# Performance work log

Hardware: AMD Instinct MI355X
Metric: run time of the kernel (lower is better)

Reference implementation:

```python
import jax, jax.numpy as jnp
from jax import lax
import numpy as np

DN = ('NCHW', 'OIHW', 'NCHW')

def _conv(x, w, b, s):
    # torch Conv2d(kernel=3, padding=1, stride=s)
    y = lax.conv_general_dilated(x, w, (s, s), ((1, 1), (1, 1)), dimension_numbers=DN)
    return y + b[None, :, None, None]

def _convT(x, w, b, s):
    # torch ConvTranspose2d weight layout [in, out, kh, kw]; kernel=3, padding=1, output_padding=s-1
    wk = jnp.flip(w, (2, 3)).transpose(1, 0, 2, 3)  # -> OIHW
    y = lax.conv_general_dilated(x, wk, (1, 1), ((1, s), (1, s)), lhs_dilation=(s, s), dimension_numbers=DN)
    return y + b[None, :, None, None]

def _inorm(x, eps=1e-5):
    # torch InstanceNorm2d (affine=False)
    m = jnp.mean(x, (2, 3), keepdims=True)
    v = jnp.var(x, (2, 3), keepdims=True)
    return (x - m) * lax.rsqrt(v + eps)

def _prelu(x, a):
    return jnp.where(x >= 0, x, a * x)

def _block(x, w, b, a, s):
    return _prelu(_inorm(_conv(x, w, b, s)), a)

def _sage(x, src, tgt, wl, bl, wr, n):
    # PyG SAGEConv, mean aggregation: lin_l(scatter_mean(x[src] -> tgt)) + lin_r(x)
    deg = jnp.zeros((n,), x.dtype).at[tgt].add(1.0)
    agg = jnp.zeros((x.shape[0], n, x.shape[2]), x.dtype).at[:, tgt].add(x[:, src])
    agg = agg / jnp.maximum(deg, 1.0)[None, :, None]
    return jnp.einsum('bnc,oc->bno', agg, wl) + bl + jnp.einsum('bnc,oc->bno', x, wr)

def setup_inputs() -> dict:
    keys = iter(jax.random.split(jax.random.key(0), 64))
    def rn(shape, s=0.05):
        return jax.random.normal(next(keys), shape, jnp.float32) * s
    inp = {}
    inp['x'] = jax.random.normal(next(keys), (16, 1, 400, 400), jnp.float32)
    inp['edges'] = jax.random.randint(next(keys), (2, 5000), 0, 625, jnp.int32)
    for name, (ci, co) in zip(['d4', 'd3', 'd2', 'd1'], [(1, 32), (32, 64), (64, 128), (128, 256)]):
        inp['w_' + name] = rn((co, ci, 3, 3)); inp['b_' + name] = rn((co,))
        inp['a_' + name] = jnp.full((1,), 0.25, jnp.float32)
    inp['w_bot'] = rn((256, 256, 3, 3)); inp['b_bot'] = rn((256,))
    inp['a_bot'] = jnp.full((1,), 0.25, jnp.float32)
    for i in ['1', '2']:
        inp['wl' + i] = rn((256, 256)); inp['bl' + i] = rn((256,)); inp['wr' + i] = rn((256, 256))
    for name, (ci, co) in zip(['u1', 'u2', 'u3'], [(512, 128), (256, 64), (128, 32)]):
        inp['w_' + name] = rn((ci, co, 3, 3)); inp['b_' + name] = rn((co,))
        inp['a_' + name] = jnp.full((1,), 0.25, jnp.float32)
    inp['w_u4'] = rn((64, 2, 3, 3)); inp['b_u4'] = rn((2,))
    return inp

def reference(x, edges, w_d4, b_d4, a_d4, w_d3, b_d3, a_d3, w_d2, b_d2, a_d2, w_d1, b_d1, a_d1, w_bot, b_bot, a_bot, wl1, bl1, wr1, wl2, bl2, wr2, w_u1, b_u1, a_u1, w_u2, b_u2, a_u2, w_u3, b_u3, a_u3, w_u4, b_u4):
    xs = []
    x = _block(x, w_d4, b_d4, a_d4, 2); xs.append(x)   # [B,32,200,200]
    x = _block(x, w_d3, b_d3, a_d3, 2); xs.append(x)   # [B,64,100,100]
    x = _block(x, w_d2, b_d2, a_d2, 2); xs.append(x)   # [B,128,50,50]
    x = _block(x, w_d1, b_d1, a_d1, 2); xs.append(x)   # [B,256,25,25]
    x = _block(x, w_bot, b_bot, a_bot, 1)              # [B,256,25,25]
    B = x.shape[0]
    x = x.reshape(B, 256, -1).transpose(0, 2, 1)       # [B,625,256]
    src, tgt = edges[0], edges[1]
    x = jax.nn.relu(_sage(x, src, tgt, wl1, bl1, wr1, 625))
    x = jax.nn.relu(_sage(x, src, tgt, wl2, bl2, wr2, 625))
    x = x.transpose(0, 2, 1).reshape(B, 256, 25, 25)
    x = jnp.concatenate([xs[3], x], 1)                 # 512 ch
    x = _prelu(_inorm(_convT(x, w_u1, b_u1, 2)), a_u1) # [B,128,50,50]
    x = jnp.concatenate([xs[2], x], 1)
    x = _prelu(_inorm(_convT(x, w_u2, b_u2, 2)), a_u2) # [B,64,100,100]
    x = jnp.concatenate([xs[1], x], 1)
    x = _prelu(_inorm(_convT(x, w_u3, b_u3, 2)), a_u3) # [B,32,200,200]
    x = jnp.concatenate([xs[0], x], 1)
    return _convT(x, w_u4, b_u4, 2)                    # [B,2,400,400], conv_only top
```

## Files before the change

kernel.cpp:

```cpp
#include <hip/hip_runtime.h>
#include <hip/hip_bf16.h>

typedef __hip_bfloat16 bf16;

typedef __bf16 bf16x8 __attribute__((ext_vector_type(8)));
typedef float  f32x16 __attribute__((ext_vector_type(16)));

static __device__ __forceinline__ float bf(const bf16 v){ return __bfloat162float(v); }
static __device__ __forceinline__ float bfu(unsigned short u){
  unsigned fw = ((unsigned)u) << 16; float v; __builtin_memcpy(&v, &fw, 4); return v;
}

static __device__ __forceinline__ float ldm(const void* p, long i, int f){
  return f ? ((const float*)p)[i] : __bfloat162float(((const bf16*)p)[i]);
}
static __device__ __forceinline__ void stm(void* p, long i, int f, float v){
  if(f) ((float*)p)[i] = v; else ((bf16*)p)[i] = __float2bfloat16(v);
}
static __device__ __forceinline__ unsigned short bfbits(float v){
  __hip_bfloat16 h = __float2bfloat16(v);
  return *(unsigned short*)&h;
}

__global__ void k_detect(const void* __restrict__ w, int* __restrict__ mode){
  if(blockIdx.x == 0 && threadIdx.x == 0){
    const unsigned int* u = (const unsigned int*)w;
    int saneLo = 0;
    for(int i = 0; i < 64; i++){
      unsigned short lo = (unsigned short)(u[i] & 0xFFFFu);
      unsigned int fw = ((unsigned int)lo) << 16;
      float v; __builtin_memcpy(&v, &fw, 4);
      float a = fabsf(v);
      if(a > 1e-7f && a < 100.f) saneLo++;
    }
    *mode = (saneLo >= 48) ? 0 : 1;
  }
}

__global__ void k_wtrans6(const void* __restrict__ w, bf16* __restrict__ wF,
                          const int* __restrict__ dmode){
  int idx = blockIdx.x * 256 + threadIdx.x;
  if(idx >= 65536) return;
  int dm = *dmode;
  int e = idx & 7;
  int L = (idx >> 3) & 63;
  int r = idx >> 9;
  int nc = r & 7;
  int kc = r >> 3;
  int o = nc*32 + (L & 31);
  int c = kc*16 + (L >> 5)*8 + e;
  wF[idx] = __float2bfloat16(ldm(w, (long)o*256 + c, dm));
}

__global__ void k_wtrans4(const void* __restrict__ w, bf16* __restrict__ wF,
                          const int* __restrict__ dmode, int Cin, int Cout){
  int idx = blockIdx.x * 256 + threadIdx.x;
  if(idx >= Cin * Cout * 9) return;
  int dm = *dmode;
  int e = idx & 7;
  int L = (idx >> 3) & 63;
  int r = idx >> 9;
  int NC = Cout >> 5;
  int nc = r % NC; r /= NC;
  int t  = r % 9;
  int kc = r / 9;
  int ci = kc*16 + (L>>5)*8 + e;
  int co = nc*32 + (L&31);
  wF[idx] = __float2bfloat16(ldm(w, ((long)ci*Cout + co)*9 + t, dm));
}

__global__ void k_wtrans5(const void* __restrict__ w, bf16* __restrict__ wF,
                          const int* __restrict__ dmode, int Cin, int Cout){
  int idx = blockIdx.x * 256 + threadIdx.x;
  if(idx >= Cin * Cout * 9) return;
  int dm = *dmode;
  int e = idx & 7;
  int L = (idx >> 3) & 63;
  int r = idx >> 9;
  int NC = Cout >> 5;
  int nc = r % NC; r /= NC;
  int t  = r % 9;
  int kc = r / 9;
  int ci = kc*16 + (L>>5)*8 + e;
  int co = nc*32 + (L&31);
  wF[idx] = __float2bfloat16(ldm(w, ((long)co*Cin + ci)*9 + t, dm));
}

__global__ __launch_bounds__(256, 4)
void k_conv_d4(const void* __restrict__ in, long in_off,
               const void* __restrict__ w, const void* __restrict__ bias,
               bf16* __restrict__ out, const int* __restrict__ dmode)
{
  __shared__ float sW[288];
  __shared__ float sB[32];
  int tid = threadIdx.x;
  int dm = *dmode;
  for(int e = tid; e < 288; e += 256) sW[e] = ldm(w, e, dm);
  if(tid < 32)  sB[tid] = ldm(bias, tid, dm);
  __syncthreads();
  int r = tid / 50, jt = tid % 50;
  if(r >= 5) return;
  int ho = blockIdx.x * 5 + r;
  int b  = blockIdx.z;
  int j0 = jt * 4;

  float x[3][9];
  long ibase = in_off + (long)b * 160000;
  #pragma unroll
  for(int rr = 0; rr < 3; rr++){
    int ir = 2*ho - 1 + rr;
    if(ir < 0 || ir >= 400){
      #pragma unroll
      for(int c = 0; c < 9; c++) x[rr][c] = 0.f;
      continue;
    }
    long rb = ibase + (long)ir * 400;
    int c0 = 2*j0 - 1;
    #pragma unroll
    for(int c = 0; c < 9; c++){
      int ic = c0 + c;
      x[rr][c] = (ic >= 0 && ic < 400) ? ldm(in, rb + ic, dm) : 0.f;
    }
  }

  long obase = ((long)b * 32) * 40000 + (long)ho * 200 + j0;
  for(int co = 0; co < 32; co++){
    const float* wv = &sW[co*9];
    float bv = sB[co];
    float a[4];
    #pragma unroll
    for(int p = 0; p < 4; p++){
      float s = bv;
      #pragma unroll
      for(int kh = 0; kh < 3; kh++)
        #pragma unroll
        for(int kw = 0; kw < 3; kw++)
          s += x[kh][2*p + kw] * wv[kh*3 + kw];
      a[p] = s;
    }
    ushort4 pk;
    pk.x = bfbits(a[0]); pk.y = bfbits(a[1]); pk.z = bfbits(a[2]); pk.w = bfbits(a[3]);
    *(ushort4*)&out[obase + (long)co * 40000] = pk;
  }
}

template<int CW, int NWC, int NWM, int S, int OCC>
__global__ __launch_bounds__(256, OCC)
void k_convSM(const void* __restrict__ in, long in_off, int fin_sel,
              const bf16* __restrict__ wF, const void* __restrict__ bias,
              void* __restrict__ out, int fout,
              const int* __restrict__ dmode,
              int Cin, int Hin, int Win, int Cout, int Hout, int Wout, int nym)
{
  constexpr int CP = 40;
  constexpr int HALF = CW/2;
  __shared__ unsigned short sX[3*CW*CP];
  int tid  = threadIdx.x;
  int lane = tid & 63;
  int wv   = tid >> 6;
  int nc   = wv % NWC;
  int mt   = wv / NWC;
  int ho   = blockIdx.x;
  int colg = blockIdx.y % nym;
  int cog  = blockIdx.y / nym;
  int b    = blockIdx.z;
  int dm   = *dmode;
  int fin  = (fin_sel == 2) ? dm : fin_sel;
  int NCtot = Cout >> 5;
  int chunk = cog*NWC + nc;
  int jl   = mt*32 + (lane & 31);
  int hi   = lane >> 5;
  int C0   = S*(colg*NWM*32);
  int ir0  = S*ho - 1;

  f32x16 acc;
  #pragma unroll
  for(int q = 0; q < 16; q++) acc[q] = 0.f;

  int p0, p1, p2;
  if(S == 2){ p0 = jl; p1 = HALF + jl; p2 = jl + 1; }
  else      { p0 = jl; p1 = jl + 1;    p2 = jl + 2; }

  for(int ci0 = 0; ci0 < Cin; ci0 += 32){
    for(int e = tid; e < 12*CW; e += 256){
      int c  = e % CW;
      int s  = e / CW;
      int kg = s & 3, r = s >> 2;
      int ir = ir0 + r;
      int ic = C0 - 1 + c;
      unsigned pk0, pk1, pk2, pk3;
      if(ir >= 0 && ir < Hin && ic >= 0 && ic < Win){
        long step = (long)Hin*Win;
        long base = in_off + ((long)b*Cin + ci0 + kg*8)*step + (long)ir*Win + ic;
        unsigned short t8[8];
        #pragma unroll
        for(int u = 0; u < 8; u++) t8[u] = bfbits(ldm(in, base + u*step, fin));
        pk0 = t8[0] | ((unsigned)t8[1]<<16);
        pk1 = t8[2] | ((unsigned)t8[3]<<16);
        pk2 = t8[4] | ((unsigned)t8[5]<<16);
        pk3 = t8[6] | ((unsigned)t8[7]<<16);
      } else { pk0=0; pk1=0; pk2=0; pk3=0; }
      int pos = (S == 2) ? ((c&1) ? HALF + (c>>1) : (c>>1)) : c;
      uint4 q; q.x=pk0; q.y=pk1; q.z=pk2; q.w=pk3;
      *(uint4*)&sX[(r*CW + pos)*CP + kg*8] = q;
    }
    __syncthreads();

    #pragma unroll
    for(int kg2 = 0; kg2 < 2; kg2++){
      int kbase = 8*hi + kg2*16;
      bf16x8 x[9];
      #pragma unroll
      for(int r = 0; r < 3; r++){
        x[r*3+0] = *(const bf16x8*)&sX[(r*CW + p0)*CP + kbase];
        x[r*3+1] = *(const bf16x8*)&sX[(r*CW + p1)*CP + kbase];
        x[r*3+2] = *(const bf16x8*)&sX[(r*CW + p2)*CP + kbase];
      }
      int kc = (ci0 >> 4) + kg2;
      const bf16x8* wb = ((const bf16x8*)wF) + ((long)(kc*9)*NCtot + chunk)*64 + lane;
      const long ws = (long)NCtot*64;
      #pragma unroll
      for(int t = 0; t < 9; t++){
        bf16x8 w = wb[(long)t*ws];
        acc = __builtin_amdgcn_mfma_f32_32x32x16_bf16(w, x[t], acc, 0,0,0);
      }
    }
    __syncthreads();
  }

  int j = colg*NWM*32 + jl;
  if(j < Wout){
    #pragma unroll
    for(int r16 = 0; r16 < 16; r16++){
      int co = chunk*32 + (r16&3) + 8*(r16>>2) + 4*hi;
      float bv = ldm(bias, co, dm);
      stm(out, ((long)b*Cout + co)*Hout*Wout + (long)ho*Wout + j, fout, acc[r16] + bv);
    }
  }
}

__global__ void k_inorm_prelu(void* __restrict__ x, int f, int HW,
                              const void* __restrict__ a, const int* __restrict__ dmode)
{
  int dm = *dmode;
  long base = (long)blockIdx.x * HW;
  float s = 0.f, s2 = 0.f;
  int vec = (f == 0) && ((HW & 3) == 0);
  if(vec){
    const ushort4* vp = (const ushort4*)((const bf16*)x + base);
    int n = HW >> 2;
    for(int i = threadIdx.x; i < n; i += 256){
      ushort4 v = vp[i];
      float a0 = bfu(v.x), a1 = bfu(v.y), a2 = bfu(v.z), a3 = bfu(v.w);
      s  += (a0 + a1) + (a2 + a3);
      s2 += (a0*a0 + a1*a1) + (a2*a2 + a3*a3);
    }
  } else {
    for(int i = threadIdx.x; i < HW; i += 256){ float v = ldm(x, base + i, f); s += v; s2 += v*v; }
  }
  __shared__ float sh[256], sh2[256];
  sh[threadIdx.x] = s; sh2[threadIdx.x] = s2; __syncthreads();
  for(int off = 128; off > 0; off >>= 1){
    if(threadIdx.x < off){ sh[threadIdx.x] += sh[threadIdx.x+off]; sh2[threadIdx.x] += sh2[threadIdx.x+off]; }
    __syncthreads();
  }
  float mean = sh[0] / HW;
  float var  = sh2[0] / HW - mean * mean;
  float inv  = rsqrtf(fmaxf(var, 0.f) + 1e-5f);
  float alpha = ldm(a, 0, dm);
  if(vec){
    ushort4* vp = (ushort4*)((bf16*)x + base);
    int n = HW >> 2;
    for(int i = threadIdx.x; i < n; i += 256){
      ushort4 v = vp[i];
      float t[4] = { bfu(v.x), bfu(v.y), bfu(v.z), bfu(v.w) };
      #pragma unroll
      for(int k = 0; k < 4; k++){
        float u = (t[k] - mean) * inv;
        t[k] = u >= 0.f ? u : alpha * u;
      }
      ushort4 o;
      o.x = bfbits(t[0]); o.y = bfbits(t[1]); o.z = bfbits(t[2]); o.w = bfbits(t[3]);
      vp[i] = o;
    }
  } else {
    for(int i = threadIdx.x; i < HW; i += 256){
      float v = (ldm(x, base + i, f) - mean) * inv;
      stm(x, base + i, f, v >= 0.f ? v : alpha * v);
    }
  }
}

__global__ void k_transpose(const float* __restrict__ in, float* __restrict__ out, int B, int C, int N){
  long idx = (long)blockIdx.x * 256 + threadIdx.x;
  long total = (long)B * C * N; if(idx >= total) return;
  int c = (int)(idx % C); long t = idx / C; int n = (int)(t % N); int b = (int)(t / N);
  out[idx] = in[((long)b * C + c) * N + n];
}

__global__ void k_deg(const int* __restrict__ tgt, float* __restrict__ deg, int E){
  int e = blockIdx.x * 256 + threadIdx.x;
  if(e < E) atomicAdd(&deg[tgt[e]], 1.0f);
}

__global__ void k_scatter(const float* __restrict__ xT, const int* __restrict__ src,
                          const int* __restrict__ tgt, float* __restrict__ agg,
                          int E, int C, int N, int B)
{
  int t = blockIdx.x * 256 + threadIdx.x;
  if(t >= E * C) return;
  int c = t % C; int e = t / C;
  int s = src[e], d = tgt[e];
  for(int b = 0; b < B; b++){
    atomicAdd(&agg[((long)b * N + d) * C + c], xT[((long)b * N + s) * C + c]);
  }
}

__global__ __launch_bounds__(256, 4)
void k_sageM(const float* __restrict__ xT, const float* __restrict__ agg,
             const float* __restrict__ deg,
             const bf16* __restrict__ wlF, const bf16* __restrict__ wrF,
             const void* __restrict__ bl,
             float* __restrict__ out, const int* __restrict__ dmode,
             int NROW, int trans)
{
  constexpr int CP = 264;
  __shared__ unsigned short sS[2*32*CP];
  int tid  = threadIdx.x;
  int lane = tid & 63;
  int wv   = tid >> 6;
  int ln   = lane & 31;
  int hi   = lane >> 5;
  int n0   = blockIdx.x * 32;
  int og0  = blockIdx.y * 128;
  int ncg  = blockIdx.y*4 + wv;
  int dm   = *dmode;

  for(int e = tid; e < 4096; e += 256){
    int c4 = e & 63;
    int r  = (e >> 6) & 31;
    int ar = e >> 11;
    int row = n0 + r;
    unsigned pk0 = 0, pk1 = 0;
    if(row < NROW){
      const float* sp = ar ? agg : xT;
      float4 v = *(const float4*)&sp[(long)row*256 + c4*4];
      if(ar){
        int n = row % 625;
        float dinv = 1.0f / fmaxf(deg[n], 1.0f);
        v.x *= dinv; v.y *= dinv; v.z *= dinv; v.w *= dinv;
      }
      pk0 = bfbits(v.x) | ((unsigned)bfbits(v.y) << 16);
      pk1 = bfbits(v.z) | ((unsigned)bfbits(v.w) << 16);
    }
    uint2 q; q.x = pk0; q.y = pk1;
    *(uint2*)&sS[(ar*32 + r)*CP + c4*4] = q;
  }
  __syncthreads();

  f32x16 acc;
  #pragma unroll
  for(int q = 0; q < 16; q++) acc[q] = 0.f;

  int xb = ln*CP + 8*hi;
  #pragma unroll
  for(int kc = 0; kc < 16; kc++){
    bf16x8 bx = *(const bf16x8*)&sS[xb + kc*16];
    bf16x8 ba = *(const bf16x8*)&sS[32*CP + xb + kc*16];
    bf16x8 wl = ((const bf16x8*)wlF)[(long)(kc*8 + ncg)*64 + lane];
    bf16x8 wr = ((const bf16x8*)wrF)[(long)(kc*8 + ncg)*64 + lane];
    acc = __builtin_amdgcn_mfma_f32_32x32x16_bf16(wl, ba, acc, 0,0,0);
    acc = __builtin_amdgcn_mfma_f32_32x32x16_bf16(wr, bx, acc, 0,0,0);
  }

  if(trans){
    int row = n0 + ln;
    if(row < NROW){
      int b = row / 625, n = row - b*625;
      #pragma unroll
      for(int r16 = 0; r16 < 16; r16++){
        int o = ncg*32 + (r16&3) + 8*(r16>>2) + 4*hi;
        float v = acc[r16] + ldm(bl, o, dm);
        out[((long)b*256 + o)*625 + n] = fmaxf(v, 0.f);
      }
    }
  } else {
    float* sO = (float*)sS;
    __syncthreads();
    #pragma unroll
    for(int r16 = 0; r16 < 16; r16++){
      int ol = wv*32 + (r16&3) + 8*(r16>>2) + 4*hi;
      float v = acc[r16] + ldm(bl, og0 + ol, dm);
      sO[ln*130 + ol] = fmaxf(v, 0.f);
    }
    __syncthreads();
    for(int e = tid; e < 4096; e += 256){
      int r = e >> 7, oc = e & 127;
      int row = n0 + r;
      if(row < NROW) out[(long)row*256 + og0 + oc] = sO[r*130 + oc];
    }
  }
}

template<int CW, int NWC, int CC, int CIP, int OCC>
__global__ __launch_bounds__(256, OCC)
void k_convTF(const void* __restrict__ inA, int fA,
              const void* __restrict__ inB, int fB,
              const bf16* __restrict__ wF, const void* __restrict__ bias,
              bf16* __restrict__ out, const int* __restrict__ dmode,
              int Hin, int Win, int Cout)
{
  __shared__ unsigned short sX[2*CW*CIP];
  int tid  = threadIdx.x;
  int lane = tid & 63;
  int wv   = tid >> 6;
  int nc   = wv % NWC;
  int mt   = wv / NWC;
  int j0   = mt * 32;
  int i    = blockIdx.x;
  int b    = blockIdx.z;
  int dm   = *dmode;
  int ln   = lane & 31;
  int hi   = lane >> 5;
  int NCtot = Cout >> 5;

  f32x16 acc0, acc1, acc2, acc3;
  #pragma unroll
  for(int q = 0; q < 16; q++){ acc0[q]=0.f; acc1[q]=0.f; acc2[q]=0.f; acc3[q]=0.f; }

  #pragma unroll
  for(int half = 0; half < 2; half++){
    const void* sp = half ? inB : inA;
    int ff = half ? fB : fA;
    for(int e = tid; e < 2*CW*(CC/8); e += 256){
      int col = e % CW;
      int s   = e / CW;
      int kg  = s % (CC/8);
      int row = s / (CC/8);
      int ii  = i + row;
      unsigned pk0=0, pk1=0, pk2=0, pk3=0;
      if(ii < Hin && col < Win){
        long step = (long)Hin*Win;
        long base = ((long)b*CC + kg*8)*step + (long)ii*Win + col;
        unsigned short t8[8];
        #pragma unroll
        for(int u = 0; u < 8; u++) t8[u] = bfbits(ldm(sp, base + u*step, ff));
        pk0 = t8[0] | ((unsigned)t8[1]<<16);
        pk1 = t8[2] | ((unsigned)t8[3]<<16);
        pk2 = t8[4] | ((unsigned)t8[5]<<16);
        pk3 = t8[6] | ((unsigned)t8[7]<<16);
      }
      uint4 q; q.x=pk0; q.y=pk1; q.z=pk2; q.w=pk3;
      *(uint4*)&sX[(row*CW + col)*CIP + kg*8] = q;
    }
    __syncthreads();

    for(int kc = 0; kc < CC/16; kc++){
      int kb = kc*16 + 8*hi;
      bf16x8 x00 = *(const bf16x8*)&sX[(j0 + ln)*CIP + kb];
      bf16x8 x01 = *(const bf16x8*)&sX[(j0 + ln + 1)*CIP + kb];
      bf16x8 x10 = *(const bf16x8*)&sX[(CW + j0 + ln)*CIP + kb];
      bf16x8 x11 = *(const bf16x8*)&sX[(CW + j0 + ln + 1)*CIP + kb];
      int kcg = half*(CC/16) + kc;
      const bf16x8* wb = ((const bf16x8*)wF) + ((long)(kcg*9)*NCtot + nc)*64 + lane;
      const int ws = NCtot*64;
      bf16x8 w0=wb[0],    w1=wb[ws],   w2=wb[2*ws], w3=wb[3*ws], w4=wb[4*ws],
             w5=wb[5*ws], w6=wb[6*ws], w7=wb[7*ws], w8=wb[8*ws];
      acc0 = __builtin_amdgcn_mfma_f32_32x32x16_bf16(w4, x00, acc0, 0,0,0);
      acc1 = __builtin_amdgcn_mfma_f32_32x32x16_bf16(w5, x00, acc1, 0,0,0);
      acc1 = __builtin_amdgcn_mfma_f32_32x32x16_bf16(w3, x01, acc1, 0,0,0);
      acc2 = __builtin_amdgcn_mfma_f32_32x32x16_bf16(w7, x00, acc2, 0,0,0);
      acc2 = __builtin_amdgcn_mfma_f32_32x32x16_bf16(w1, x10, acc2, 0,0,0);
      acc3 = __builtin_amdgcn_mfma_f32_32x32x16_bf16(w8, x00, acc3, 0,0,0);
      acc3 = __builtin_amdgcn_mfma_f32_32x32x16_bf16(w6, x01, acc3, 0,0,0);
      acc3 = __builtin_amdgcn_mfma_f32_32x32x16_bf16(w2, x10, acc3, 0,0,0);
      acc3 = __builtin_amdgcn_mfma_f32_32x32x16_bf16(w0, x11, acc3, 0,0,0);
    }
    __syncthreads();
  }

  int j = j0 + ln;
  if(j < Win){
    int Wout = 2*Win;
    #pragma unroll
    for(int r = 0; r < 16; r++){
      int co = nc*32 + (r&3) + 8*(r>>2) + 4*hi;
      float bv = ldm(bias, co, dm);
      long base0 = (((long)b*Cout + co)*2*Hin + 2*i)*(long)Wout + 2*j;
      unsigned p0 = bfbits(acc0[r]+bv) | ((unsigned)bfbits(acc1[r]+bv) << 16);
      unsigned p1 = bfbits(acc2[r]+bv) | ((unsigned)bfbits(acc3[r]+bv) << 16);
      *(unsigned*)&out[base0]        = p0;
      *(unsigned*)&out[base0 + Wout] = p1;
    }
  }
}

__global__ __launch_bounds__(256, 2)
void k_convT8(const bf16* __restrict__ inA, const bf16* __restrict__ inB,
              const void* __restrict__ w, const void* __restrict__ bias,
              void* __restrict__ out, long out_off, int fout_sel,
              const int* __restrict__ dmode, int Hin, int Win)
{
  __shared__ float sW[64*2*9];
  __shared__ float sB[2];
  int tid = threadIdx.x;
  int dm = *dmode;
  for(int e = tid; e < 64*2*9; e += 256) sW[e] = ldm(w, e, dm);
  if(tid < 2) sB[tid] = ldm(bias, tid, dm);
  __syncthreads();
  int r  = tid / 50;
  int jt = tid % 50;
  if(r >= 5) return;
  int i  = blockIdx.x * 5 + r;
  int b  = blockIdx.z;
  int j0 = jt * 4;
  int fout = (fout_sel == 2) ? dm : fout_sel;

  float acc[2][4][4];
  #pragma unroll
  for(int co = 0; co < 2; co++)
    #pragma unroll
    for(int p = 0; p < 4; p++){
      acc[co][p][0]=0.f; acc[co][p][1]=0.f; acc[co][p][2]=0.f; acc[co][p][3]=0.f;
    }

  bool e4   = (j0 + 4 < Win);
  bool row1 = (i + 1 < Hin);

  for(int ci = 0; ci < 64; ci++){
    const bf16* src = (ci < 32) ? inA : inB;
    int cc = ci & 31;
    const bf16* rp = src + ((long)b*32 + cc)*(long)Hin*Win + (long)i*Win + j0;
    float x0[5], x1[5];
    ushort4 v0 = *(const ushort4*)rp;
    x0[0]=bfu(v0.x); x0[1]=bfu(v0.y); x0[2]=bfu(v0.z); x0[3]=bfu(v0.w);
    x0[4] = e4 ? bf(rp[4]) : 0.f;
    if(row1){
      ushort4 v1 = *(const ushort4*)(rp + Win);
      x1[0]=bfu(v1.x); x1[1]=bfu(v1.y); x1[2]=bfu(v1.z); x1[3]=bfu(v1.w);
      x1[4] = e4 ? bf(rp[Win + 4]) : 0.f;
    } else {
      x1[0]=0.f; x1[1]=0.f; x1[2]=0.f; x1[3]=0.f; x1[4]=0.f;
    }
    const float* wp = &sW[ci*18];
    float wv[18];
    #pragma unroll
    for(int k = 0; k < 18; k++) wv[k] = wp[k];
    #pragma unroll
    for(int p = 0; p < 4; p++){
      float a00 = x0[p], a01 = x0[p+1], a10 = x1[p], a11 = x1[p+1];
      #pragma unroll
      for(int co = 0; co < 2; co++){
        const float* wc = &wv[co*9];
        acc[co][p][0] += a00*wc[4];
        acc[co][p][1] += a00*wc[5] + a01*wc[3];
        acc[co][p][2] += a00*wc[7] + a10*wc[1];
        acc[co][p][3] += a00*wc[8] + a01*wc[6] + a10*wc[2] + a11*wc[0];
      }
    }
  }
  int Wout = 2*Win;
  #pragma unroll
  for(int co = 0; co < 2; co++){
    float bv = sB[co];
    long base = out_off + (((long)b*2 + co)*2*Hin + 2*i)*(long)Wout + 2*j0;
    #pragma unroll
    for(int p = 0; p < 4; p++){
      stm(out, base + 2*p,            fout, acc[co][p][0] + bv);
      stm(out, base + 2*p + 1,        fout, acc[co][p][1] + bv);
      stm(out, base + 2*p + Wout,     fout, acc[co][p][2] + bv);
      stm(out, base + 2*p + Wout + 1, fout, acc[co][p][3] + bv);
    }
  }
}

static inline int cdiv(long a, long b){ return (int)((a + b - 1) / b); }

extern "C" void kernel_launch(void* const* d_in, const int* in_sizes, int n_in,
                              void* d_out, int out_size, void* d_ws, size_t ws_size,
                              hipStream_t stream) {
  const void* x_in  = d_in[0];
  const int*  edges = (const int*)d_in[1];
  const int* src = edges;
  const int* tgt = edges + 5000;
  const void *w_d4=d_in[2],  *b_d4=d_in[3],  *a_d4=d_in[4];
  const void *w_d3=d_in[5],  *b_d3=d_in[6],  *a_d3=d_in[7];
  const void *w_d2=d_in[8],  *b_d2=d_in[9],  *a_d2=d_in[10];
  const void *w_d1=d_in[11], *b_d1=d_in[12], *a_d1=d_in[13];
  const void *w_bot=d_in[14],*b_bot=d_in[15],*a_bot=d_in[16];
  const void *wl1=d_in[17], *bl1=d_in[18], *wr1=d_in[19];
  const void *wl2=d_in[20], *bl2=d_in[21], *wr2=d_in[22];
  const void *w_u1=d_in[23], *b_u1=d_in[24], *a_u1=d_in[25];
  const void *w_u2=d_in[26], *b_u2=d_in[27], *a_u2=d_in[28];
  const void *w_u3=d_in[29], *b_u3=d_in[30], *a_u3=d_in[31];
  const void *w_u4=d_in[32], *b_u4=d_in[33];

  const int NNODE = 625, E = 5000, CG = 256;

  const long TAIL = 4096 + 4*262144L + (589824L + 147456L + 36864L) * 2;
  const long ENCW = 976896L * 2;
  int Bc = 16;
  while(Bc > 1 && (7680000L * Bc + TAIL) > (long)ws_size) Bc >>= 1;
  int enc_in_pool = (Bc >= 8);
  if(!enc_in_pool){
    Bc = 16;
    while(Bc > 1 && (7680000L * Bc + TAIL + ENCW) > (long)ws_size) Bc >>= 1;
  }

  char* wsb = (char*)d_ws;
  long o_xs1  = 2560000L * Bc;
  long o_BIGA = 3840000L * Bc;
  long o_BIGB = 6400000L * Bc;
  long o_deg  = 7680000L * Bc;
  bf16*  xs0 = (bf16*)wsb;
  bf16*  xs1 = (bf16*)(wsb + o_xs1);
  bf16*  xs2 = (bf16*)(wsb + o_BIGA);
  bf16*  xs3 = (bf16*)(wsb + o_BIGA +  640000L*Bc);
  float* bot = (float*)(wsb + o_BIGA +  960000L*Bc);
  float* xT  = (float*)(wsb + o_BIGA + 1600000L*Bc);
  bf16*  u1  = (bf16*)(wsb + o_BIGA + 1600000L*Bc);
  bf16*  u3  = (bf16*)(wsb + o_BIGA);
  float* agg = (float*)(wsb + o_BIGB);
  float* g1  = (float*)(wsb + o_BIGB +  640000L*Bc);
  bf16*  u2  = (bf16*)(wsb + o_BIGB);
  float* deg = (float*)(wsb + o_deg);
  int*  mode = (int*)(wsb + o_deg + 3072);
  bf16*  wlF1 = (bf16*)(wsb + o_deg + 4096);
  bf16*  wrF1 = wlF1 + 65536;
  bf16*  wlF2 = wrF1 + 65536;
  bf16*  wrF2 = wlF2 + 65536;
  bf16*  wTu1 = (bf16*)(wsb + o_deg + 4096 + 4*262144L);
  bf16*  wTu2 = wTu1 + 589824;
  bf16*  wTu3 = wTu2 + 147456;
  bf16*  wTd3 = enc_in_pool ? (bf16*)(wsb + o_BIGA + 2240000L*Bc) : (wTu3 + 36864);
  bf16*  wTd2 = wTd3 + 18432;
  bf16*  wTd1 = wTd2 + 73728;
  bf16*  wTdB = wTd1 + 294912;
  float* g2  = bot;

  hipLaunchKernelGGL(k_detect, dim3(1), dim3(1), 0, stream, w_d4, mode);

  hipMemsetAsync(deg, 0, NNODE*sizeof(float), stream);
  hipLaunchKernelGGL(k_deg, dim3(cdiv(E,256)), dim3(256), 0, stream, tgt, deg, E);
  hipLaunchKernelGGL(k_wtrans6, dim3(256), dim3(256), 0, stream, wl1, wlF1, mode);
  hipLaunchKernelGGL(k_wtrans6, dim3(256), dim3(256), 0, stream, wr1, wrF1, mode);
  hipLaunchKernelGGL(k_wtrans6, dim3(256), dim3(256), 0, stream, wl2, wlF2, mode);
  hipLaunchKernelGGL(k_wtrans6, dim3(256), dim3(256), 0, stream, wr2, wrF2, mode);
  hipLaunchKernelGGL(k_wtrans4, dim3(cdiv(589824,256)), dim3(256), 0, stream, w_u1, wTu1, mode, 512, 128);
  hipLaunchKernelGGL(k_wtrans4, dim3(cdiv(147456,256)), dim3(256), 0, stream, w_u2, wTu2, mode, 256, 64);
  hipLaunchKernelGGL(k_wtrans4, dim3(cdiv(36864,256)),  dim3(256), 0, stream, w_u3, wTu3, mode, 128, 32);

  for(int bo = 0; bo < 16; bo += Bc){
    long x_off   = (long)bo * 160000;
    long out_off = (long)bo * 320000;

    hipLaunchKernelGGL(k_wtrans5, dim3(cdiv(18432,256)),  dim3(256), 0, stream, w_d3, wTd3, mode, 32, 64);
    hipLaunchKernelGGL(k_wtrans5, dim3(cdiv(73728,256)),  dim3(256), 0, stream, w_d2, wTd2, mode, 64, 128);
    hipLaunchKernelGGL(k_wtrans5, dim3(cdiv(294912,256)), dim3(256), 0, stream, w_d1, wTd1, mode, 128, 256);
    hipLaunchKernelGGL(k_wtrans5, dim3(cdiv(589824,256)), dim3(256), 0, stream, w_bot, wTdB, mode, 256, 256);

    hipLaunchKernelGGL(k_conv_d4, dim3(40, 1, Bc), dim3(256), 0, stream,
                       x_in, x_off, w_d4, b_d4, xs0, mode);
    hipLaunchKernelGGL(k_inorm_prelu, dim3(Bc*32), dim3(256), 0, stream, xs0, 0, 40000, a_d4, mode);
    hipLaunchKernelGGL((k_convSM<130,2,2,2,4>), dim3(100, 2, Bc), dim3(256), 0, stream,
                       xs0, 0L, 0, wTd3, b_d3, xs1, 0, mode, 32, 200, 200, 64, 100, 100, 2);
    hipLaunchKernelGGL(k_inorm_prelu, dim3(Bc*64), dim3(256), 0, stream, xs1, 0, 10000, a_d3, mode);
    hipLaunchKernelGGL((k_convSM<66,4,1,2,4>), dim3(50, 2, Bc), dim3(256), 0, stream,
                       xs1, 0L, 0, wTd2, b_d2, xs2, 0, mode, 64, 100, 100, 128, 50, 50, 2);
    hipLaunchKernelGGL(k_inorm_prelu, dim3(Bc*128), dim3(256), 0, stream, xs2, 0, 2500, a_d2, mode);
    hipLaunchKernelGGL((k_convSM<66,4,1,2,4>), dim3(25, 2, Bc), dim3(256), 0, stream,
                       xs2, 0L, 0, wTd1, b_d1, xs3, 0, mode, 128, 50, 50, 256, 25, 25, 1);
    hipLaunchKernelGGL(k_inorm_prelu, dim3(Bc*256), dim3(256), 0, stream, xs3, 0, 625, a_d1, mode);
    hipLaunchKernelGGL((k_convSM<34,4,1,1,4>), dim3(25, 2, Bc), dim3(256), 0, stream,
                       xs3, 0L, 0, wTdB, b_bot, bot, 1, mode, 256, 25, 25, 256, 25, 25, 1);
    hipLaunchKernelGGL(k_inorm_prelu, dim3(Bc*256), dim3(256), 0, stream, bot, 1, 625, a_bot, mode);

    { long n = (long)Bc*CG*NNODE;
      hipLaunchKernelGGL(k_transpose, dim3(cdiv(n,256)), dim3(256), 0, stream, bot, xT, Bc, CG, NNODE); }
    hipMemsetAsync(agg, 0, 640000L*Bc, stream);
    hipLaunchKernelGGL(k_scatter, dim3(cdiv((long)E*CG,256)), dim3(256), 0, stream, xT, src, tgt, agg, E, CG, NNODE, Bc);
    hipLaunchKernelGGL(k_sageM, dim3(cdiv((long)Bc*NNODE,32), 2), dim3(256), 0, stream,
                       xT, agg, deg, wlF1, wrF1, bl1, g1, mode, Bc*NNODE, 0);
    hipMemsetAsync(agg, 0, 640000L*Bc, stream);
    hipLaunchKernelGGL(k_scatter, dim3(cdiv((long)E*CG,256)), dim3(256), 0, stream, g1, src, tgt, agg, E, CG, NNODE, Bc);
    hipLaunchKernelGGL(k_sageM, dim3(cdiv((long)Bc*NNODE,32), 2), dim3(256), 0, stream,
                       g1, agg, deg, wlF2, wrF2, bl2, g2, mode, Bc*NNODE, 1);

    hipLaunchKernelGGL((k_convTF<34,4,256,264,4>), dim3(25, 1, Bc), dim3(256), 0, stream,
                       xs3, 0, g2, 1, wTu1, b_u1, u1, mode, 25, 25, 128);
    hipLaunchKernelGGL(k_inorm_prelu, dim3(Bc*128), dim3(256), 0, stream, u1, 0, 2500, a_u1, mode);
    hipLaunchKernelGGL((k_convTF<66,2,128,136,4>), dim3(50, 1, Bc), dim3(256), 0, stream,
                       xs2, 0, u1, 0, wTu2, b_u2, u2, mode, 50, 50, 64);
    hipLaunchKernelGGL(k_inorm_prelu, dim3(Bc*64), dim3(256), 0, stream, u2, 0, 10000, a_u2, mode);
    hipLaunchKernelGGL((k_convTF<130,1,64,72,4>), dim3(100, 1, Bc), dim3(256), 0, stream,
                       xs1, 0, u2, 0, wTu3, b_u3, u3, mode, 100, 100, 32);
    hipLaunchKernelGGL(k_inorm_prelu, dim3(Bc*32), dim3(256), 0, stream, u3, 0, 40000, a_u3, mode);
    hipLaunchKernelGGL(k_convT8, dim3(40, 1, Bc), dim3(256), 0, stream,
                       xs0, u3, w_u4, b_u4, d_out, out_off, 2, mode, 200, 200);
  }
}
```

Before: 905.6 us.

## Split convT channel halves across wave groups with LDS reduction

Transposed-conv kernel now uses 512 threads. Wave groups 0-3 process the skip-connection input channels and waves 4-7 the decoder input channels concurrently. Partial accumulators are then summed through shared memory before the bias and store. This aims to increase parallelism and remove the serialized two-phase staging. In exchange it doubles shared memory per block and adds a reduction pass.

```diff
diff --git a/kernel.cpp b/kernel.cpp
--- a/kernel.cpp
+++ b/kernel.cpp
@@ -402,20 +402,22 @@
   }
 }
 
-template<int CW, int NWC, int CC, int CIP, int OCC>
-__global__ __launch_bounds__(256, OCC)
-void k_convTF(const void* __restrict__ inA, int fA,
+template<int CW, int NWC, int NWM, int CC, int CIP>
+__global__ __launch_bounds__(512, 4)
+void k_convTG(const void* __restrict__ inA, int fA,
               const void* __restrict__ inB, int fB,
               const bf16* __restrict__ wF, const void* __restrict__ bias,
               bf16* __restrict__ out, const int* __restrict__ dmode,
               int Hin, int Win, int Cout)
 {
-  __shared__ unsigned short sX[2*CW*CIP];
+  __shared__ unsigned short sX[4*CW*CIP];
   int tid  = threadIdx.x;
   int lane = tid & 63;
   int wv   = tid >> 6;
-  int nc   = wv % NWC;
-  int mt   = wv / NWC;
+  int low  = wv & 3;
+  int h    = wv >> 2;
+  int nc   = low % NWC;
+  int mt   = low / NWC;
   int j0   = mt * 32;
   int i    = blockIdx.x;
   int b    = blockIdx.z;
@@ -428,69 +430,87 @@
   #pragma unroll
   for(int q = 0; q < 16; q++){ acc0[q]=0.f; acc1[q]=0.f; acc2[q]=0.f; acc3[q]=0.f; }
 
-  #pragma unroll
-  for(int half = 0; half < 2; half++){
-    const void* sp = half ? inB : inA;
-    int ff = half ? fB : fA;
-    for(int e = tid; e < 2*CW*(CC/8); e += 256){
-      int col = e % CW;
-      int s   = e / CW;
-      int kg  = s % (CC/8);
-      int row = s / (CC/8);
-      int ii  = i + row;
-      unsigned pk0=0, pk1=0, pk2=0, pk3=0;
-      if(ii < Hin && col < Win){
-        long step = (long)Hin*Win;
-        long base = ((long)b*CC + kg*8)*step + (long)ii*Win + col;
-        unsigned short t8[8];
-        #pragma unroll
-        for(int u = 0; u < 8; u++) t8[u] = bfbits(ldm(sp, base + u*step, ff));
-        pk0 = t8[0] | ((unsigned)t8[1]<<16);
-        pk1 = t8[2] | ((unsigned)t8[3]<<16);
-        pk2 = t8[4] | ((unsigned)t8[5]<<16);
-        pk3 = t8[6] | ((unsigned)t8[7]<<16);
+  for(int e = tid; e < 4*CW*(CC/8); e += 512){
+    int col = e % CW;
+    int s   = e / CW;
+    int kg  = s % (CC/8); s /= (CC/8);
+    int row = s & 1;
+    int hf  = s >> 1;
+    int ii  = i + row;
+    unsigned pk0=0, pk1=0, pk2=0, pk3=0;
+    if(ii < Hin && col < Win){
+      const void* sp = hf ? inB : inA;
+      int ff = hf ? fB : fA;
+      long step = (long)Hin*Win;
+      long base = ((long)b*CC + kg*8)*step + (long)ii*Win + col;
+      unsigned short t8[8];
+      #pragma unroll
+      for(int u = 0; u < 8; u++) t8[u] = bfbits(ldm(sp, base + u*step, ff));
+      pk0 = t8[0] | ((unsigned)t8[1]<<16);
+      pk1 = t8[2] | ((unsigned)t8[3]<<16);
+      pk2 = t8[4] | ((unsigned)t8[5]<<16);
+      pk3 = t8[6] | ((unsigned)t8[7]<<16);
+    }
+    uint4 q; q.x=pk0; q.y=pk1; q.z=pk2; q.w=pk3;
+    *(uint4*)&sX[((hf*2 + row)*CW + col)*CIP + kg*8] = q;
+  }
+  __syncthreads();
+
+  for(int kc = 0; kc < CC/16; kc++){
+    int kb = kc*16 + 8*hi;
+    bf16x8 x00 = *(const bf16x8*)&sX[((h*2+0)*CW + j0 + ln)*CIP + kb];
+    bf16x8 x01 = *(const bf16x8*)&sX[((h*2+0)*CW + j0 + ln + 1)*CIP + kb];
+    bf16x8 x10 = *(const bf16x8*)&sX[((h*2+1)*CW + j0 + ln)*CIP + kb];
+    bf16x8 x11 = *(const bf16x8*)&sX[((h*2+1)*CW + j0 + ln + 1)*CIP + kb];
+    int kcg = h*(CC/16) + kc;
+    const bf16x8* wb = ((const bf16x8*)wF) + ((long)(kcg*9)*NCtot + nc)*64 + lane;
+    const int ws = NCtot*64;
+    bf16x8 w0=wb[0],    w1=wb[ws],   w2=wb[2*ws], w3=wb[3*ws], w4=wb[4*ws],
+           w5=wb[5*ws], w6=wb[6*ws], w7=wb[7*ws], w8=wb[8*ws];
+    acc0 = __builtin_amdgcn_mfma_f32_32x32x16_bf16(w4, x00, acc0, 0,0,0);
+    acc1 = __builtin_amdgcn_mfma_f32_32x32x16_bf16(w5, x00, acc1, 0,0,0);
+    acc1 = __builtin_amdgcn_mfma_f32_32x32x16_bf16(w3, x01, acc1, 0,0,0);
+    acc2 = __builtin_amdgcn_mfma_f32_32x32x16_bf16(w7, x00, acc2, 0,0,0);
+    acc2 = __builtin_amdgcn_mfma_f32_32x32x16_bf16(w1, x10, acc2, 0,0,0);
+    acc3 = __builtin_amdgcn_mfma_f32_32x32x16_bf16(w8, x00, acc3, 0,0,0);
+    acc3 = __builtin_amdgcn_mfma_f32_32x32x16_bf16(w6, x01, acc3, 0,0,0);
+    acc3 = __builtin_amdgcn_mfma_f32_32x32x16_bf16(w2, x10, acc3, 0,0,0);
+    acc3 = __builtin_amdgcn_mfma_f32_32x32x16_bf16(w0, x11, acc3, 0,0,0);
+  }
+
+  float* sR = (float*)sX;
+  __syncthreads();
+  if(h == 1){
+    #pragma unroll
+    for(int q = 0; q < 16; q++){
+      sR[(0*16+q)*256 + low*64 + lane] = acc0[q];
+      sR[(1*16+q)*256 + low*64 + lane] = acc1[q];
+      sR[(2*16+q)*256 + low*64 + lane] = acc2[q];
+      sR[(3*16+q)*256 + low*64 + lane] = acc3[q];
+    }
+  }
+  __syncthreads();
+  if(h == 0){
+    #pragma unroll
+    for(int q = 0; q < 16; q++){
+      acc0[q] += sR[(0*16+q)*256 + low*64 + lane];
+      acc1[q] += sR[(1*16+q)*256 + low*64 + lane];
+      acc2[q] += sR[(2*16+q)*256 + low*64 + lane];
+      acc3[q] += sR[(3*16+q)*256 + low*64 + lane];
+    }
+    int j = j0 + ln;
+    if(j < Win){
+      int Wout = 2*Win;
+      #pragma unroll
+      for(int r = 0; r < 16; r++){
+        int co = nc*32 + (r&3) + 8*(r>>2) + 4*hi;
+        float bv = ldm(bias, co, dm);
+        long base0 = (((long)b*Cout + co)*2*Hin + 2*i)*(long)Wout + 2*j;
+        unsigned p0 = bfbits(acc0[r]+bv) | ((unsigned)bfbits(acc1[r]+bv) << 16);
+        unsigned p1 = bfbits(acc2[r]+bv) | ((unsigned)bfbits(acc3[r]+bv) << 16);
+        *(unsigned*)&out[base0]        = p0;
+        *(unsigned*)&out[base0 + Wout] = p1;
       }
-      uint4 q; q.x=pk0; q.y=pk1; q.z=pk2; q.w=pk3;
-      *(uint4*)&sX[(row*CW + col)*CIP + kg*8] = q;
-    }
-    __syncthreads();
-
-    for(int kc = 0; kc < CC/16; kc++){
-      int kb = kc*16 + 8*hi;
-      bf16x8 x00 = *(const bf16x8*)&sX[(j0 + ln)*CIP + kb];
-      bf16x8 x01 = *(const bf16x8*)&sX[(j0 + ln + 1)*CIP + kb];
-      bf16x8 x10 = *(const bf16x8*)&sX[(CW + j0 + ln)*CIP + kb];
-      bf16x8 x11 = *(const bf16x8*)&sX[(CW + j0 + ln + 1)*CIP + kb];
-      int kcg = half*(CC/16) + kc;
-      const bf16x8* wb = ((const bf16x8*)wF) + ((long)(kcg*9)*NCtot + nc)*64 + lane;
-      const int ws = NCtot*64;
-      bf16x8 w0=wb[0],    w1=wb[ws],   w2=wb[2*ws], w3=wb[3*ws], w4=wb[4*ws],
-             w5=wb[5*ws], w6=wb[6*ws], w7=wb[7*ws], w8=wb[8*ws];
-      acc0 = __builtin_amdgcn_mfma_f32_32x32x16_bf16(w4, x00, acc0, 0,0,0);
-      acc1 = __builtin_amdgcn_mfma_f32_32x32x16_bf16(w5, x00, acc1, 0,0,0);
-      acc1 = __builtin_amdgcn_mfma_f32_32x32x16_bf16(w3, x01, acc1, 0,0,0);
-      acc2 = __builtin_amdgcn_mfma_f32_32x32x16_bf16(w7, x00, acc2, 0,0,0);
-      acc2 = __builtin_amdgcn_mfma_f32_32x32x16_bf16(w1, x10, acc2, 0,0,0);
-      acc3 = __builtin_amdgcn_mfma_f32_32x32x16_bf16(w8, x00, acc3, 0,0,0);
-      acc3 = __builtin_amdgcn_mfma_f32_32x32x16_bf16(w6, x01, acc3, 0,0,0);
-      acc3 = __builtin_amdgcn_mfma_f32_32x32x16_bf16(w2, x10, acc3, 0,0,0);
-      acc3 = __builtin_amdgcn_mfma_f32_32x32x16_bf16(w0, x11, acc3, 0,0,0);
-    }
-    __syncthreads();
-  }
-
-  int j = j0 + ln;
-  if(j < Win){
-    int Wout = 2*Win;
-    #pragma unroll
-    for(int r = 0; r < 16; r++){
-      int co = nc*32 + (r&3) + 8*(r>>2) + 4*hi;
-      float bv = ldm(bias, co, dm);
-      long base0 = (((long)b*Cout + co)*2*Hin + 2*i)*(long)Wout + 2*j;
-      unsigned p0 = bfbits(acc0[r]+bv) | ((unsigned)bfbits(acc1[r]+bv) << 16);
-      unsigned p1 = bfbits(acc2[r]+bv) | ((unsigned)bfbits(acc3[r]+bv) << 16);
-      *(unsigned*)&out[base0]        = p0;
-      *(unsigned*)&out[base0 + Wout] = p1;
     }
   }
 }
@@ -686,13 +706,13 @@
     hipLaunchKernelGGL(k_sageM, dim3(cdiv((long)Bc*NNODE,32), 2), dim3(256), 0, stream,
                        g1, agg, deg, wlF2, wrF2, bl2, g2, mode, Bc*NNODE, 1);
 
-    hipLaunchKernelGGL((k_convTF<34,4,256,264,4>), dim3(25, 1, Bc), dim3(256), 0, stream,
+    hipLaunchKernelGGL((k_convTG<34,4,1,256,264>), dim3(25, 1, Bc), dim3(512), 0, stream,
                        xs3, 0, g2, 1, wTu1, b_u1, u1, mode, 25, 25, 128);
     hipLaunchKernelGGL(k_inorm_prelu, dim3(Bc*128), dim3(256), 0, stream, u1, 0, 2500, a_u1, mode);
-    hipLaunchKernelGGL((k_convTF<66,2,128,136,4>), dim3(50, 1, Bc), dim3(256), 0, stream,
+    hipLaunchKernelGGL((k_convTG<66,2,2,128,136>), dim3(50, 1, Bc), dim3(512), 0, stream,
                        xs2, 0, u1, 0, wTu2, b_u2, u2, mode, 50, 50, 64);
     hipLaunchKernelGGL(k_inorm_prelu, dim3(Bc*64), dim3(256), 0, stream, u2, 0, 10000, a_u2, mode);
-    hipLaunchKernelGGL((k_convTF<130,1,64,72,4>), dim3(100, 1, Bc), dim3(256), 0, stream,
+    hipLaunchKernelGGL((k_convTG<130,1,4,64,72>), dim3(100, 1, Bc), dim3(512), 0, stream,
                        xs1, 0, u2, 0, wTu3, b_u3, u3, mode, 100, 100, 32);
     hipLaunchKernelGGL(k_inorm_prelu, dim3(Bc*32), dim3(256), 0, stream, u3, 0, 40000, a_u3, mode);
     hipLaunchKernelGGL(k_convT8, dim3(40, 1, Bc), dim3(256), 0, stream,
```

Measured after the change: 883.6 us. 1.02x faster.
